# Kernel tuning notes

Hardware: AMD Instinct MI355X
Metric: run time of the kernel (lower is better)

Reference implementation:

```python
import jax, jax.numpy as jnp
import numpy as np

B, C, H, W = 16, 256, 64, 64
K = 1024


def setup_inputs() -> dict:
    key = jax.random.key(0)
    k1, k2 = jax.random.split(key)
    z = jax.random.normal(k1, (B, C, H, W), dtype=jnp.float32)
    codebook = jax.random.normal(k2, (K, C), dtype=jnp.float32)
    return {"z": z, "codebook": codebook}


def reference(z, codebook):
    # assign: nearest-code indices via squared euclidean distance
    b, c, h, w = z.shape
    zf = jnp.transpose(z, (0, 2, 3, 1)).reshape(-1, c)            # [N, C]
    # ||z||^2 - 2 z.cb^T + ||cb||^2  -> [N, K]
    dists = (jnp.sum(zf * zf, axis=1, keepdims=True)
             - 2.0 * jnp.einsum('nc,kc->nk', zf, codebook)
             + jnp.sum(codebook * codebook, axis=1)[None, :])
    idx = jnp.argmin(dists, axis=1)                                # [N]
    indices = idx.reshape(b, 1, h, w)                              # [B,1,H,W]
    # embed_code: gather codebook rows, back to BCHW
    zq = codebook[idx].reshape(b, h, w, c)                         # [B,H,W,C]
    zq = jnp.transpose(zq, (0, 3, 1, 2))                           # [B,C,H,W]
    return zq, indices
```

## Files before the change

### kernel.cpp

```cpp
#include <hip/hip_runtime.h>


#define HWSZ 4096
#define CDIM 256
#define KCODES 1024
#define NPIX 65536
#define ZQ_ELEMS (16 * 256 * 4096)
#define MARGIN 0.75f

#define WS_CBSWZ 0
#define WS_CBN64 524288
#define WS_CBN32 532480
#define WS_CNT   536576
#define WS_LISTS 536592

#define L_NRM    65536
#define L_MK     69632
#define L_SBEST  72704
#define L_FLP    73216
#define L_FLQ    73728
#define L_LCNT   74240
#define L_TOTAL  74496

typedef __attribute__((ext_vector_type(8))) short bf16x8;
typedef __attribute__((ext_vector_type(4))) float f32x4;
typedef __attribute__((ext_vector_type(4))) unsigned short us4;

#define MFMA16(a, b, c) __builtin_amdgcn_mfma_f32_16x16x32_bf16(a, b, c, 0, 0, 0)

__device__ __forceinline__ unsigned short f2bf(float f) {
  unsigned u = __float_as_uint(f);
  unsigned r = u + 0x7FFFu + ((u >> 16) & 1u);
  return (unsigned short)(r >> 16);
}

__device__ __forceinline__ unsigned cvtpk(float lo, float hi) {
  unsigned r;
  asm("v_cvt_pk_bf16_f32 %0, %1, %2" : "=v"(r) : "v"(lo), "v"(hi));
  return r;
}

__device__ __forceinline__ void gload_lds16(const void* g, void* l) {
  __builtin_amdgcn_global_load_lds(
      (const __attribute__((address_space(1))) unsigned int*)g,
      (__attribute__((address_space(3))) unsigned int*)l, 16, 0, 0);
}

__device__ __forceinline__ void ins3(unsigned& k1, unsigned& k2, unsigned& k3,
                                     unsigned k) {
  unsigned nk2, nk3;
  asm("v_med3_u32 %0, %1, %2, %3" : "=v"(nk2) : "v"(k1), "v"(k2), "v"(k));
  asm("v_med3_u32 %0, %1, %2, %3" : "=v"(nk3) : "v"(k2), "v"(k3), "v"(k));
  k1 = k1 < k ? k1 : k;
  k2 = nk2;
  k3 = nk3;
}

__device__ __forceinline__ float keyf(unsigned k) {
  return __uint_as_float(k & 0xFFFFFC00u);
}

__global__ void vq_prep(const float* __restrict__ cb,
                        unsigned short* __restrict__ cbswz,
                        double* __restrict__ cbn64,
                        float* __restrict__ cbn32p,
                        int* __restrict__ cnt) {
  const int t = threadIdx.x;
  if (blockIdx.x == 0 && t == 0) { cnt[0] = 0; cnt[1] = 0; }
  const int code = blockIdx.x * 4 + (t >> 6);
  const int lane = t & 63;
  const int c4 = lane * 4;

  float4 v = *(const float4*)(cb + (size_t)code * CDIM + c4);
  us4 hv;
  hv.x = f2bf(-2.f * v.x); hv.y = f2bf(-2.f * v.y);
  hv.z = f2bf(-2.f * v.z); hv.w = f2bf(-2.f * v.w);
  const int K = (code >> 9) * 32 + ((code >> 4) & 31);
  const int kk = c4 >> 5;
  const int lg = (c4 >> 3) & 3;
  const int within = (c4 & 7) * 2;
  size_t off = (size_t)K * 8192 + kk * 1024 + (code & 15) * 64 + lg * 16 + within;
  *(us4*)((char*)cbswz + off) = hv;

  double s = (double)v.x * v.x;
  s = fma((double)v.y, (double)v.y, s);
  s = fma((double)v.z, (double)v.z, s);
  s = fma((double)v.w, (double)v.w, s);
#pragma unroll
  for (int o = 32; o; o >>= 1) s += __shfl_xor(s, o, 64);
  if (lane == 0) {
    cbn64[code] = s;
    cbn32p[code] = (float)s + 512.0f;
  }
}

__launch_bounds__(256, 2)
__global__ void vq_stage1(const float* __restrict__ z,
                          const float* __restrict__ cb,
                          const unsigned short* __restrict__ cbswz,
                          const float* __restrict__ cbn32p,
                          float* __restrict__ out_zq,
                          float* __restrict__ out_idx,
                          int* __restrict__ cnt,
                          int* __restrict__ listA, int capA,
                          int* __restrict__ listB, int capB,
                          float* __restrict__ zws, int zcap) {
  extern __shared__ char smem[];
  const int t = threadIdx.x;
  const int w = t >> 6;
  const int lane = t & 63;
  const int lg = lane >> 4;
  const int lcode = lane & 15;
  const int h = w >> 1;
  const int q = w & 1;
  const int p0 = blockIdx.x * 128;
  const int b = p0 >> 12;
  const int hw0 = p0 & (HWSZ - 1);
  const float* zb = z + (size_t)b * (CDIM * HWSZ) + hw0;

  char* const bb0 = smem + q * 8192;
  char* const bb1 = smem + 16384 + q * 8192;
  char* const bb2 = smem + 32768 + q * 8192;
  char* const bb3 = smem + 49152 + q * 8192;
  float* nrm = (float*)(smem + L_NRM);

  const int stl = h * 4096 + lane * 16;
  const char* cbbase = (const char*)cbswz + (size_t)q * 262144 + stl;

#define STAGE(CIDX, SBUF)                                             \
  {                                                                   \
    const char* gs_ = cbbase + ((size_t)(CIDX) << 13);                \
    char* ld_ = (SBUF) + stl;                                         \
    gload_lds16(gs_, ld_);                                            \
    gload_lds16(gs_ + 1024, ld_ + 1024);                              \
    gload_lds16(gs_ + 2048, ld_ + 2048);                              \
    gload_lds16(gs_ + 3072, ld_ + 3072);                              \
  }

  STAGE(0, bb0);
  STAGE(1, bb1);
  STAGE(2, bb2);

  bf16x8 af[4][8];
#pragma unroll
  for (int T = 0; T < 4; ++T) {
    const float* zr = zb + (h * 64 + T * 16 + lcode);
#pragma unroll
    for (int kk = 0; kk < 8; ++kk) {
      const int ch0 = kk * 32 + lg * 8;
      float v0 = zr[(size_t)(ch0 + 0) * HWSZ];
      float v1 = zr[(size_t)(ch0 + 1) * HWSZ];
      float v2 = zr[(size_t)(ch0 + 2) * HWSZ];
      float v3 = zr[(size_t)(ch0 + 3) * HWSZ];
      float v4 = zr[(size_t)(ch0 + 4) * HWSZ];
      float v5 = zr[(size_t)(ch0 + 5) * HWSZ];
      float v6 = zr[(size_t)(ch0 + 6) * HWSZ];
      float v7 = zr[(size_t)(ch0 + 7) * HWSZ];
      unsigned p01 = cvtpk(v0, v1);
      unsigned p23 = cvtpk(v2, v3);
      unsigned p45 = cvtpk(v4, v5);
      unsigned p67 = cvtpk(v6, v7);
      bf16x8 f;
      f[0] = (short)(p01 & 0xFFFF); f[1] = (short)(p01 >> 16);
      f[2] = (short)(p23 & 0xFFFF); f[3] = (short)(p23 >> 16);
      f[4] = (short)(p45 & 0xFFFF); f[5] = (short)(p45 >> 16);
      f[6] = (short)(p67 & 0xFFFF); f[7] = (short)(p67 >> 16);
      af[T][kk] = f;
    }
  }

  *(float4*)(nrm + t * 4) = *(const float4*)(cbn32p + t * 4);
  __syncthreads();

  unsigned k1[4][4], k2[4][4], k3[4][4];
#pragma unroll
  for (int T = 0; T < 4; ++T)
#pragma unroll
    for (int q4 = 0; q4 < 4; ++q4) {
      k1[T][q4] = 0xFFFFFFFFu; k2[T][q4] = 0xFFFFFFFFu; k3[T][q4] = 0xFFFFFFFFu;
    }

  const int bq = lcode * 64 + lg * 16;
  const float* nrmp = nrm + q * 512 + lcode;
  const int kbase = q * 512 + lcode;
  float cnn = nrmp[0];

#define BODY(CIDX, RBUF, SBUF, DOSTAGE, WN)                           \
  {                                                                   \
    asm volatile("s_waitcnt vmcnt(" WN ")" ::: "memory");             \
    __builtin_amdgcn_s_barrier();                                     \
    __builtin_amdgcn_sched_barrier(0);                                \
    const float cn_ = cnn;                                            \
    if ((CIDX) < 31) cnn = nrmp[((CIDX) + 1) * 16];                   \
    if (DOSTAGE) STAGE((CIDX) + 3, SBUF);                             \
    const char* pb_ = (RBUF) + bq;                                    \
    f32x4 a0 = {cn_, cn_, cn_, cn_};                                  \
    f32x4 a1 = {cn_, cn_, cn_, cn_};                                  \
    f32x4 a2 = {cn_, cn_, cn_, cn_};                                  \
    f32x4 a3 = {cn_, cn_, cn_, cn_};                                  \
    __builtin_amdgcn_s_setprio(1);                                    \
    _Pragma("unroll")                                                 \
    for (int kk = 0; kk < 8; ++kk) {                                  \
      bf16x8 bf_ = *(const bf16x8*)(pb_ + kk * 1024);                 \
      a0 = MFMA16(af[0][kk], bf_, a0);                                \
      a1 = MFMA16(af[1][kk], bf_, a1);                                \
      a2 = MFMA16(af[2][kk], bf_, a2);                                \
      a3 = MFMA16(af[3][kk], bf_, a3);                                \
    }                                                                 \
    __builtin_amdgcn_s_setprio(0);                                    \
    const unsigned code_ = (unsigned)(kbase + (CIDX) * 16);           \
    _Pragma("unroll")                                                 \
    for (int q4 = 0; q4 < 4; ++q4) {                                  \
      ins3(k1[0][q4], k2[0][q4], k3[0][q4],                           \
           (__float_as_uint(a0[q4]) & 0xFFFFFC00u) | code_);          \
      ins3(k1[1][q4], k2[1][q4], k3[1][q4],                           \
           (__float_as_uint(a1[q4]) & 0xFFFFFC00u) | code_);          \
      ins3(k1[2][q4], k2[2][q4], k3[2][q4],                           \
           (__float_as_uint(a2[q4]) & 0xFFFFFC00u) | code_);          \
      ins3(k1[3][q4], k2[3][q4], k3[3][q4],                           \
           (__float_as_uint(a3[q4]) & 0xFFFFFC00u) | code_);          \
    }                                                                 \
  }

#pragma unroll 1
  for (int c4 = 0; c4 < 28; c4 += 4) {
    BODY(c4 + 0, bb0, bb3, 1, "8");
    BODY(c4 + 1, bb1, bb0, 1, "8");
    BODY(c4 + 2, bb2, bb1, 1, "8");
    BODY(c4 + 3, bb3, bb2, 1, "8");
  }
  BODY(28, bb0, bb3, 1, "8");
  BODY(29, bb1, bb0, 0, "8");
  BODY(30, bb2, bb1, 0, "4");
  BODY(31, bb3, bb2, 0, "0");
#undef BODY
#undef STAGE

#pragma unroll
  for (int mask = 1; mask <= 8; mask <<= 1) {
#pragma unroll
    for (int T = 0; T < 4; ++T)
#pragma unroll
      for (int q4 = 0; q4 < 4; ++q4) {
        unsigned o1 = __shfl_xor(k1[T][q4], mask, 64);
        unsigned o2 = __shfl_xor(k2[T][q4], mask, 64);
        unsigned o3 = __shfl_xor(k3[T][q4], mask, 64);
        ins3(k1[T][q4], k2[T][q4], k3[T][q4], o1);
        ins3(k1[T][q4], k2[T][q4], k3[T][q4], o2);
        ins3(k1[T][q4], k2[T][q4], k3[T][q4], o3);
      }
  }

  unsigned* mk = (unsigned*)(smem + L_MK);
  int* sbest = (int*)(smem + L_SBEST);
  int* flp = (int*)(smem + L_FLP);
  int* flq = (int*)(smem + L_FLQ);
  int* lcnt = (int*)(smem + L_LCNT);
  if (t == 0) *lcnt = 0;
  if (lcode == 0) {
#pragma unroll
    for (int T = 0; T < 4; ++T)
#pragma unroll
      for (int q4 = 0; q4 < 4; ++q4) {
        int row = h * 64 + T * 16 + lg * 4 + q4;
        unsigned* d = mk + (row * 2 + q) * 3;
        d[0] = k1[T][q4]; d[1] = k2[T][q4]; d[2] = k3[T][q4];
      }
  }
  __syncthreads();

  if (t < 128) {
    unsigned a1 = mk[t * 6 + 0], a2 = mk[t * 6 + 1], a3 = mk[t * 6 + 2];
    ins3(a1, a2, a3, mk[t * 6 + 3]);
    ins3(a1, a2, a3, mk[t * 6 + 4]);
    ins3(a1, a2, a3, mk[t * 6 + 5]);
    const int p = p0 + t;
    const int i1 = (int)(a1 & 1023u);
    sbest[t] = i1;
    out_idx[p] = (float)i1;
    float f1 = keyf(a1);
    float g2 = keyf(a2) - f1;
    float g3 = keyf(a3) - f1;
    if (g3 < MARGIN) {
      int pos = atomicAdd(cnt + 1, 1);
      if (pos < capB) listB[pos] = p;
    } else if (g2 < MARGIN) {
      int pos = atomicAdd(cnt, 1);
      if (pos < capA) {
        listA[2 * pos] = p | (i1 << 16);
        listA[2 * pos + 1] = (int)(a2 & 1023u) | ((int)(a3 & 1023u) << 16);
        if (pos < zcap) {
          int li = atomicAdd(lcnt, 1);
          flp[li] = p;
          flq[li] = pos;
        }
      }
    }
  }
  __syncthreads();

  {
    const int px = t & 127;
    const int best = sbest[px];
    const int ch0g = (t >> 7) * 128;
    const float* crow = cb + (size_t)best * CDIM + ch0g;
    float* ob = out_zq + (size_t)b * (CDIM * HWSZ) + (size_t)ch0g * HWSZ + hw0 + px;
#pragma unroll 4
    for (int c2 = 0; c2 < 128; c2 += 4) {
      float4 v = *(const float4*)(crow + c2);
      ob[(size_t)(c2 + 0) * HWSZ] = v.x;
      ob[(size_t)(c2 + 1) * HWSZ] = v.y;
      ob[(size_t)(c2 + 2) * HWSZ] = v.z;
      ob[(size_t)(c2 + 3) * HWSZ] = v.w;
    }
  }

  {
    const int nf = *lcnt;
    for (int e = 0; e < nf; ++e) {
      const int p = flp[e];
      const int slot = flq[e];
      const int bb = p >> 12;
      const int hh = p & (HWSZ - 1);
      zws[(size_t)slot * 256 + t] =
          z[(size_t)bb * (CDIM * HWSZ) + (size_t)t * HWSZ + hh];
    }
  }
}

__launch_bounds__(256)
__global__ void vq_fix(const float* __restrict__ z,
                       const float* __restrict__ cb,
                       const double* __restrict__ cbn64,
                       float* __restrict__ out_zq,
                       float* __restrict__ out_idx,
                       const int* __restrict__ cnt,
                       const int* __restrict__ listA, int capA,
                       const float* __restrict__ zws, int zcap,
                       const int* __restrict__ listB, int capB) {
  const int t = threadIdx.x;
  const int w = t >> 6;
  const int lane = t & 63;

  {
    const int wid = blockIdx.x * 4 + w;
    const int nw = gridDim.x * 4;
    int n = cnt[0];
    if (n > capA) n = capA;

    for (int i = wid; i < n; i += nw) {
      const int e0 = listA[2 * i];
      const int e1 = listA[2 * i + 1];
      const int p = e0 & 0xFFFF;
      int cand[3];
      cand[0] = (e0 >> 16) & 1023;
      cand[1] = e1 & 0xFFFF;
      cand[2] = (e1 >> 16) & 1023;
      const int b = p >> 12;
      const int hw = p & (HWSZ - 1);
      const int ch0 = lane * 4;

      double zv[4];
      if (i < zcap) {
        float4 zf = ((const float4*)(zws + (size_t)i * 256))[lane];
        zv[0] = (double)zf.x; zv[1] = (double)zf.y;
        zv[2] = (double)zf.z; zv[3] = (double)zf.w;
      } else {
        const float* zb = z + (size_t)b * (CDIM * HWSZ) + hw;
#pragma unroll
        for (int j = 0; j < 4; ++j) zv[j] = (double)zb[(size_t)(ch0 + j) * HWSZ];
      }

      double d[3];
#pragma unroll
      for (int tt = 0; tt < 3; ++tt) {
        float4 cv = *(const float4*)(cb + (size_t)cand[tt] * CDIM + ch0);
        double s = zv[0] * (double)cv.x;
        s = fma(zv[1], (double)cv.y, s);
        s = fma(zv[2], (double)cv.z, s);
        s = fma(zv[3], (double)cv.w, s);
#pragma unroll
        for (int off = 32; off; off >>= 1) s += __shfl_xor(s, off, 64);
        d[tt] = fma(-2.0, s, cbn64[cand[tt]]);
      }

      double bd = d[0];
      int bi = cand[0];
#pragma unroll
      for (int tt = 1; tt < 3; ++tt) {
        bool takes = (d[tt] < bd) || (d[tt] == bd && cand[tt] < bi);
        bd = takes ? d[tt] : bd;
        bi = takes ? cand[tt] : bi;
      }

      if (bi != cand[0]) {
        if (lane == 0) out_idx[p] = (float)bi;
        float4 cv = *(const float4*)(cb + (size_t)bi * CDIM + ch0);
        float* ob = out_zq + (size_t)b * (CDIM * HWSZ) + hw;
        ob[(size_t)(ch0 + 0) * HWSZ] = cv.x;
        ob[(size_t)(ch0 + 1) * HWSZ] = cv.y;
        ob[(size_t)(ch0 + 2) * HWSZ] = cv.z;
        ob[(size_t)(ch0 + 3) * HWSZ] = cv.w;
      }
    }
  }

  __shared__ double zl[256];
  __shared__ double sd[4];
  __shared__ int si[4];
  __shared__ int sfin;
  int n = cnt[1];
  if (n > capB) n = capB;

  for (int i = blockIdx.x; i < n; i += gridDim.x) {
    const int p = listB[i];
    const int b = p >> 12;
    const int hw = p & (HWSZ - 1);
    const float* zb = z + (size_t)b * (CDIM * HWSZ) + hw;
    zl[t] = (double)zb[(size_t)t * HWSZ];
    __syncthreads();

    const int g = t >> 2;
    const int sub = t & 3;
    const double* zq4 = zl + sub * 64;
    double bd = 1e300;
    int bi = 0;

    for (int j = 0; j < 16; ++j) {
      const int code = g + 64 * j;
      const float* crow = cb + (size_t)code * CDIM + sub * 64;
      double s = 0.0;
#pragma unroll
      for (int q4 = 0; q4 < 64; q4 += 4) {
        float4 cv = *(const float4*)(crow + q4);
        s = fma(zq4[q4 + 0], (double)cv.x, s);
        s = fma(zq4[q4 + 1], (double)cv.y, s);
        s = fma(zq4[q4 + 2], (double)cv.z, s);
        s = fma(zq4[q4 + 3], (double)cv.w, s);
      }
      s += __shfl_xor(s, 1, 64);
      s += __shfl_xor(s, 2, 64);
      double d = fma(-2.0, s, cbn64[code]);
      bool takes = (d < bd) || (d == bd && code < bi);
      bd = takes ? d : bd;
      bi = takes ? code : bi;
    }

#pragma unroll
    for (int off = 4; off <= 32; off <<= 1) {
      double od = __shfl_xor(bd, off, 64);
      int oi = __shfl_xor(bi, off, 64);
      bool takes = (od < bd) || (od == bd && oi < bi);
      bd = takes ? od : bd;
      bi = takes ? oi : bi;
    }
    if (lane == 0) { sd[w] = bd; si[w] = bi; }
    __syncthreads();
    if (t == 0) {
      double fd = sd[0];
      int fi = si[0];
#pragma unroll
      for (int k = 1; k < 4; ++k) {
        bool takes = (sd[k] < fd) || (sd[k] == fd && si[k] < fi);
        fd = takes ? sd[k] : fd;
        fi = takes ? si[k] : fi;
      }
      const int old = (int)out_idx[p];
      sfin = (fi != old) ? fi : -1;
      if (fi != old) out_idx[p] = (float)fi;
    }
    __syncthreads();
    const int best = sfin;
    if (best >= 0) {
      float* ob = out_zq + (size_t)b * (CDIM * HWSZ) + hw;
      ob[(size_t)t * HWSZ] = cb[(size_t)best * CDIM + t];
    }
    __syncthreads();
  }
}

extern "C" void kernel_launch(void* const* d_in, const int* in_sizes, int n_in,
                              void* d_out, int out_size, void* d_ws, size_t ws_size,
                              hipStream_t stream) {
  const float* z = (const float*)d_in[0];
  const float* cb = (const float*)d_in[1];
  float* out = (float*)d_out;
  float* out_zq = out;
  float* out_idx = out + ZQ_ELEMS;

  char* ws = (char*)d_ws;
  unsigned short* cbswz = (unsigned short*)(ws + WS_CBSWZ);
  double* cbn64 = (double*)(ws + WS_CBN64);
  float* cbn32p = (float*)(ws + WS_CBN32);
  int* cnt = (int*)(ws + WS_CNT);

  long long avail = (long long)ws_size - WS_LISTS;
  if (avail < 0) avail = 0;
  long long capA_ll = (avail / 4) / 8;
  if (capA_ll > NPIX) capA_ll = NPIX;
  int capA = (int)capA_ll;
  int* listA = (int*)(ws + WS_LISTS);
  long long rem = avail - (long long)capA * 8;
  long long capB_ll = rem / 8;
  if (capB_ll > NPIX) capB_ll = NPIX;
  if (capB_ll < 0) capB_ll = 0;
  int capB = (int)capB_ll;
  int* listB = (int*)(ws + WS_LISTS + (size_t)capA * 8);
  long long zoff = (WS_LISTS + (long long)capA * 8 + (long long)capB * 4 + 15) &
                   ~15LL;
  long long zcap_ll = ((long long)ws_size - zoff) / 1024;
  if (zcap_ll < 0) zcap_ll = 0;
  if (zcap_ll > capA) zcap_ll = capA;
  int zcap = (int)zcap_ll;
  float* zws = (float*)(ws + zoff);

  hipFuncSetAttribute(reinterpret_cast<const void*>(vq_stage1),
                      hipFuncAttributeMaxDynamicSharedMemorySize, L_TOTAL);

  vq_prep<<<256, 256, 0, stream>>>(cb, cbswz, cbn64, cbn32p, cnt);
  vq_stage1<<<512, 256, L_TOTAL, stream>>>(z, cb, cbswz, cbn32p, out_zq, out_idx,
                                           cnt, listA, capA, listB, capB,
                                           zws, zcap);
  vq_fix<<<256, 256, 0, stream>>>(z, cb, cbn64, out_zq, out_idx,
                                  cnt, listA, capA, zws, zcap, listB, capB);
}
```

Measured before the change: 155.0 us.

## Give each wave private double-buffered codebook tiles and drop block barriers

Replaces the block-shared four-slot LDS ring with per-wave double buffers. Each wave stages its own full 8 KB codebook tile with eight async global-to-LDS loads, which removes the per-tile s_barrier and the setprio hints. The codebook swizzle is re-laid out so each lane reads 16 contiguous bytes per k-step. The trade-off is that waves sharing a codebook half now each fetch the same tiles, doubling global/L2 traffic, and prefetch depth drops from three tiles to two.

```diff
diff --git a/kernel.cpp b/kernel.cpp
--- a/kernel.cpp
+++ b/kernel.cpp
@@ -79,7 +79,7 @@
   const int kk = c4 >> 5;
   const int lg = (c4 >> 3) & 3;
   const int within = (c4 & 7) * 2;
-  size_t off = (size_t)K * 8192 + kk * 1024 + (code & 15) * 64 + lg * 16 + within;
+  size_t off = (size_t)K * 8192 + kk * 1024 + lg * 256 + (code & 15) * 16 + within;
   *(us4*)((char*)cbswz + off) = hv;
 
   double s = (double)v.x * v.x;
@@ -118,28 +118,28 @@
   const int hw0 = p0 & (HWSZ - 1);
   const float* zb = z + (size_t)b * (CDIM * HWSZ) + hw0;
 
-  char* const bb0 = smem + q * 8192;
-  char* const bb1 = smem + 16384 + q * 8192;
-  char* const bb2 = smem + 32768 + q * 8192;
-  char* const bb3 = smem + 49152 + q * 8192;
+  char* const wbuf = smem + w * 16384;
+  char* const wb0 = wbuf;
+  char* const wb1 = wbuf + 8192;
   float* nrm = (float*)(smem + L_NRM);
 
-  const int stl = h * 4096 + lane * 16;
-  const char* cbbase = (const char*)cbswz + (size_t)q * 262144 + stl;
-
-#define STAGE(CIDX, SBUF)                                             \
+  const char* cbbase = (const char*)cbswz + (size_t)q * 262144 + lane * 16;
+
+#define STAGE(CIDX, DST)                                              \
   {                                                                   \
     const char* gs_ = cbbase + ((size_t)(CIDX) << 13);                \
-    char* ld_ = (SBUF) + stl;                                         \
-    gload_lds16(gs_, ld_);                                            \
-    gload_lds16(gs_ + 1024, ld_ + 1024);                              \
-    gload_lds16(gs_ + 2048, ld_ + 2048);                              \
-    gload_lds16(gs_ + 3072, ld_ + 3072);                              \
-  }
-
-  STAGE(0, bb0);
-  STAGE(1, bb1);
-  STAGE(2, bb2);
+    gload_lds16(gs_,        (DST));                                   \
+    gload_lds16(gs_ + 1024, (DST) + 1024);                            \
+    gload_lds16(gs_ + 2048, (DST) + 2048);                            \
+    gload_lds16(gs_ + 3072, (DST) + 3072);                            \
+    gload_lds16(gs_ + 4096, (DST) + 4096);                            \
+    gload_lds16(gs_ + 5120, (DST) + 5120);                            \
+    gload_lds16(gs_ + 6144, (DST) + 6144);                            \
+    gload_lds16(gs_ + 7168, (DST) + 7168);                            \
+  }
+
+  STAGE(0, wb0);
+  STAGE(1, wb1);
 
   bf16x8 af[4][8];
 #pragma unroll
@@ -180,25 +180,21 @@
       k1[T][q4] = 0xFFFFFFFFu; k2[T][q4] = 0xFFFFFFFFu; k3[T][q4] = 0xFFFFFFFFu;
     }
 
-  const int bq = lcode * 64 + lg * 16;
+  const int lane16 = lane * 16;
   const float* nrmp = nrm + q * 512 + lcode;
   const int kbase = q * 512 + lcode;
   float cnn = nrmp[0];
 
-#define BODY(CIDX, RBUF, SBUF, DOSTAGE, WN)                           \
+#define BODY(CIDX, RBUF, DOSTAGE, WN)                                 \
   {                                                                   \
     asm volatile("s_waitcnt vmcnt(" WN ")" ::: "memory");             \
-    __builtin_amdgcn_s_barrier();                                     \
-    __builtin_amdgcn_sched_barrier(0);                                \
     const float cn_ = cnn;                                            \
     if ((CIDX) < 31) cnn = nrmp[((CIDX) + 1) * 16];                   \
-    if (DOSTAGE) STAGE((CIDX) + 3, SBUF);                             \
-    const char* pb_ = (RBUF) + bq;                                    \
+    const char* pb_ = (RBUF) + lane16;                                \
     f32x4 a0 = {cn_, cn_, cn_, cn_};                                  \
     f32x4 a1 = {cn_, cn_, cn_, cn_};                                  \
     f32x4 a2 = {cn_, cn_, cn_, cn_};                                  \
     f32x4 a3 = {cn_, cn_, cn_, cn_};                                  \
-    __builtin_amdgcn_s_setprio(1);                                    \
     _Pragma("unroll")                                                 \
     for (int kk = 0; kk < 8; ++kk) {                                  \
       bf16x8 bf_ = *(const bf16x8*)(pb_ + kk * 1024);                 \
@@ -207,7 +203,9 @@
       a2 = MFMA16(af[2][kk], bf_, a2);                                \
       a3 = MFMA16(af[3][kk], bf_, a3);                                \
     }                                                                 \
-    __builtin_amdgcn_s_setprio(0);                                    \
+    asm volatile("s_waitcnt lgkmcnt(0)" ::: "memory");                \
+    __builtin_amdgcn_sched_barrier(0);                                \
+    if (DOSTAGE) STAGE((CIDX) + 2, RBUF);                             \
     const unsigned code_ = (unsigned)(kbase + (CIDX) * 16);           \
     _Pragma("unroll")                                                 \
     for (int q4 = 0; q4 < 4; ++q4) {                                  \
@@ -223,16 +221,12 @@
   }
 
 #pragma unroll 1
-  for (int c4 = 0; c4 < 28; c4 += 4) {
-    BODY(c4 + 0, bb0, bb3, 1, "8");
-    BODY(c4 + 1, bb1, bb0, 1, "8");
-    BODY(c4 + 2, bb2, bb1, 1, "8");
-    BODY(c4 + 3, bb3, bb2, 1, "8");
-  }
-  BODY(28, bb0, bb3, 1, "8");
-  BODY(29, bb1, bb0, 0, "8");
-  BODY(30, bb2, bb1, 0, "4");
-  BODY(31, bb3, bb2, 0, "0");
+  for (int c2 = 0; c2 < 30; c2 += 2) {
+    BODY(c2 + 0, wb0, 1, "8");
+    BODY(c2 + 1, wb1, 1, "8");
+  }
+  BODY(30, wb0, 0, "8");
+  BODY(31, wb1, 0, "0");
 #undef BODY
 #undef STAGE
 
```

Measured after the change: 154.8 us. No clear change (-0.1%).
